# Kernel tuning notes

Hardware: AMD Instinct MI355X
Metric: run time of the kernel (lower is better)

Reference implementation:

```python
import jax, jax.numpy as jnp
import numpy as np

T = 32400   # bs*H*W BEV queries (1*180*180)
S = 16896   # bs*num_cams*h*w image keys (1*6*32*88)
E = 256     # embed_dim
H = 8       # num_heads
D = 32      # head_dim
MAXL = 32   # max interval length (ref_num_f)


def _mlp(x, w1, b1, w2, b2):
    # nn.Sequential(Linear(E,2E), ReLU, Linear(2E,E))
    return jax.nn.relu(x @ w1 + b1) @ w2 + b2


def setup_inputs() -> dict:
    k0 = jax.random.key(0)
    ks = jax.random.split(k0, 8)
    # ragged interval structure: every BEV cell has an interval of length (idx%32)+1
    lengths = (np.arange(T) % MAXL) + 1
    starts = np.concatenate([np.zeros(1, np.int64), np.cumsum(lengths)[:-1]])
    N = int(lengths.sum())  # 534472 frustum points
    ranks_bev = np.repeat(np.arange(T), lengths)          # sorted by BEV cell
    rng = np.random.default_rng(0)
    ranks_feat = rng.integers(0, S, size=N)               # which key/value row each point reads

    def lin(k, fi, fo):
        return jax.random.normal(k, (fi, fo), jnp.float32) * (1.0 / np.sqrt(fi))

    key_feat = jax.random.normal(ks[1], (S, E), jnp.float32)
    return dict(
        query_depth=jax.random.normal(ks[0], (T, E), jnp.float32),
        key=key_feat,
        value=key_feat,  # module asserts torch.equal(key, value)
        q_w1=lin(ks[2], E, 2 * E), q_b1=jnp.zeros((2 * E,), jnp.float32),
        q_w2=lin(ks[3], 2 * E, E), q_b2=jnp.zeros((E,), jnp.float32),
        k_w1=lin(ks[4], E, 2 * E), k_b1=jnp.zeros((2 * E,), jnp.float32),
        k_w2=lin(ks[5], 2 * E, E), k_b2=jnp.zeros((E,), jnp.float32),
        ranks_feat_f=jnp.asarray(ranks_feat, jnp.int32),
        ranks_bev_f=jnp.asarray(ranks_bev, jnp.int32),
        interval_starts_f=jnp.asarray(starts, jnp.int32),
        interval_lengths_f=jnp.asarray(lengths, jnp.int32),
        ref_num=MAXL,
    )


def reference(query_depth, key, value,
              q_w1, q_b1, q_w2, q_b2,
              k_w1, k_b1, k_w2, k_b2,
              ranks_feat_f, ranks_bev_f,
              interval_starts_f, interval_lengths_f, ref_num):
    scaling = 1.0 / jnp.sqrt(jnp.float32(D))
    q = (_mlp(query_depth, q_w1, q_b1, q_w2, q_b2) * scaling).reshape(T, H, D)
    k = _mlp(key, k_w1, k_b1, k_w2, k_b2).reshape(S, H, D)
    v = value.reshape(S, H, D)

    N = ranks_bev_f.shape[0]
    pt = jnp.arange(N, dtype=jnp.int32)
    # interval id of each point (intervals are contiguous, sorted by start)
    iid = jnp.searchsorted(interval_starts_f, pt, side='right') - 1
    ranks_ref = pt - interval_starts_f[iid]  # within-interval slot, in [0, ref_num)

    # per-point raw attention logit: q[bev] . k[feat] per head  -> [N, H]
    w = jnp.einsum('nhd,nhd->nh', q[ranks_bev_f], k[ranks_feat_f])

    # scatter into ragged weight tensor [T, H, ref_num]; padding masked to -1e9
    attn = jnp.full((T, H, ref_num), -1e9, jnp.float32)
    attn = attn.at[ranks_bev_f, :, ranks_ref].set(w)
    attn = jax.nn.softmax(attn, axis=-1)

    # gather normalized weights back per point and scatter-combine values
    wp = attn[ranks_bev_f, :, ranks_ref]          # [N, H]
    vp = v[ranks_feat_f]                          # [N, H, D]
    out = jnp.zeros((T, H, D), jnp.float32).at[ranks_bev_f].add(wp[:, :, None] * vp)
    return out.reshape(T, E)
```

## Files before the change

### kernel.cpp

```cpp
#include <hip/hip_runtime.h>
#include <hip/hip_bf16.h>
#include <cstdint>
#include <cstddef>

constexpr int T_Q   = 32400;
constexpr int T_PAD = 32512;
constexpr int S_K   = 16896;
constexpr int E_DIM = 256;
constexpr int HID   = 512;

typedef __bf16 bf16x8 __attribute__((ext_vector_type(8)));
typedef float  f32x4  __attribute__((ext_vector_type(4)));
typedef unsigned short ushort8v __attribute__((ext_vector_type(8)));

__device__ __forceinline__ void async16(const __hip_bfloat16* gp, __hip_bfloat16* lp) {
    __builtin_amdgcn_global_load_lds(
        (const __attribute__((address_space(1))) void*)(gp),
        (__attribute__((address_space(3))) void*)(lp), 16, 0, 0);
}

__device__ __forceinline__ float b2f(unsigned short u) {
    return __uint_as_float(((unsigned)u) << 16);
}

constexpr int NB_K = (S_K * E_DIM / 4) / 256;
constexpr int NB_PREP = NB_K + 128;

__global__ __launch_bounds__(256) void prep(
    const float* __restrict__ val_in,
    const float* __restrict__ s0, const float* __restrict__ s1,
    const float* __restrict__ s2, const float* __restrict__ s3,
    __hip_bfloat16* __restrict__ kvB,
    __hip_bfloat16* __restrict__ d0, __hip_bfloat16* __restrict__ d1,
    __hip_bfloat16* __restrict__ d2, __hip_bfloat16* __restrict__ d3) {
    __shared__ float tb[64][65];
    const int b = blockIdx.x;
    const int tid = threadIdx.x;

    if (b < NB_K) {
        int i = (b * 256 + tid) * 4;
        float4 f = *(const float4*)(val_in + i);
        union { ushort4 u4; __hip_bfloat16 bb[4]; } cv;
        cv.bb[0] = __float2bfloat16(f.x);
        cv.bb[1] = __float2bfloat16(f.y);
        cv.bb[2] = __float2bfloat16(f.z);
        cv.bb[3] = __float2bfloat16(f.w);
        int r = i >> 8, c = i & 255;
        *(ushort4*)(kvB + (size_t)r * 512 + 256 + c) = cv.u4;
        return;
    }

    int tloc = b - NB_K;
    int m = tloc >> 5;
    int tt = tloc & 31;
    const float* S = m == 0 ? s0 : m == 1 ? s1 : m == 2 ? s2 : s3;
    __hip_bfloat16* D = m == 0 ? d0 : m == 1 ? d1 : m == 2 ? d2 : d3;
    int Kd, Nd, kt, nt;
    if ((m & 1) == 0) { Kd = 256; Nd = 512; kt = tt & 3; nt = tt >> 2; }
    else              { Kd = 512; Nd = 256; kt = tt & 7; nt = tt >> 3; }
    int tx = tid & 63, ty = tid >> 6;
#pragma unroll
    for (int p = 0; p < 16; ++p) {
        int row = ty * 16 + p;
        tb[row][tx] = S[(size_t)(kt * 64 + row) * Nd + nt * 64 + tx];
    }
    __syncthreads();
#pragma unroll
    for (int p = 0; p < 16; ++p) {
        int row = ty * 16 + p;
        D[(size_t)(nt * 64 + row) * Kd + kt * 64 + tx] = __float2bfloat16(tb[tx][row]);
    }
}


constexpr int MLP_QT = T_PAD / 64;
constexpr int MLP_KT = S_K / 64;
constexpr int MLP_NB = MLP_QT + MLP_KT;

__global__ __launch_bounds__(512) void mlp_fused(
    const float* __restrict__ Aq, const float* __restrict__ Ak,
    const __hip_bfloat16* __restrict__ W1q, const __hip_bfloat16* __restrict__ W1k,
    const __hip_bfloat16* __restrict__ W2q, const __hip_bfloat16* __restrict__ W2k,
    const float* __restrict__ b1q, const float* __restrict__ b1k,
    const float* __restrict__ b2q, const float* __restrict__ b2k,
    __hip_bfloat16* __restrict__ Cq, __hip_bfloat16* __restrict__ Ck,
    float scaleq, int qtiles) {
    __shared__ __hip_bfloat16 As[64 * 256];
    __shared__ __hip_bfloat16 Bs[256 * 64];
    __shared__ __hip_bfloat16 Hs[64 * 512];

    const int b = blockIdx.x;
    const bool isq = b < qtiles;
    const float* A  = isq ? Aq : Ak;
    const __hip_bfloat16* W1 = isq ? W1q : W1k;
    const __hip_bfloat16* W2 = isq ? W2q : W2k;
    const float* b1 = isq ? b1q : b1k;
    const float* b2 = isq ? b2q : b2k;
    __hip_bfloat16* C = isq ? Cq : Ck;
    const int ldc = isq ? E_DIM : 512;
    const float scale = isq ? scaleq : 1.0f;
    const int mrow0 = (isq ? b : b - qtiles) * 64;
    const int rowlim = isq ? T_Q : S_K;

    const int tid = threadIdx.x;
    const int w = tid >> 6, l = tid & 63;
    const int lm = l & 15, lq = l >> 4;
    const int wm = w >> 2;
    const int wn4 = w & 3;
    const int srow8 = l >> 3;
    const int u8 = l & 7;
    const int scolB = (u8 ^ srow8) << 3;

#pragma unroll
    for (int c = 0; c < 4; ++c) {
        int idx = tid + c * 512;
        int row = idx >> 5;
        int u = idx & 31;
        int gr = mrow0 + row;
        float4 f0 = make_float4(0.f, 0.f, 0.f, 0.f);
        float4 f1 = make_float4(0.f, 0.f, 0.f, 0.f);
        if (gr < rowlim) {
            const float* ap = A + (size_t)gr * 256 + u * 8;
            f0 = *(const float4*)ap;
            f1 = *(const float4*)(ap + 4);
        }
        union { bf16x8 v; __hip_bfloat16 bb[8]; } cv;
        cv.bb[0] = __float2bfloat16(f0.x); cv.bb[1] = __float2bfloat16(f0.y);
        cv.bb[2] = __float2bfloat16(f0.z); cv.bb[3] = __float2bfloat16(f0.w);
        cv.bb[4] = __float2bfloat16(f1.x); cv.bb[5] = __float2bfloat16(f1.y);
        cv.bb[6] = __float2bfloat16(f1.z); cv.bb[7] = __float2bfloat16(f1.w);
        int pu = (u & 24) | ((u & 7) ^ (row & 7));
        *(bf16x8*)(As + row * 256 + pu * 8) = cv.v;
    }

#pragma unroll 1
    for (int nh = 0; nh < 2; ++nh) {
        f32x4 acc[2][4] = {};
        for (int k0 = 0; k0 < 256; k0 += 64) {
#pragma unroll
            for (int c = 0; c < 4; ++c) {
                int r = w * 32 + c * 8 + srow8;
                async16(W1 + (size_t)(nh * 256 + r) * 256 + k0 + scolB,
                        Bs + (w * 32 + c * 8) * 64);
            }
            __syncthreads();
#pragma unroll
            for (int ks = 0; ks < 2; ++ks) {
                bf16x8 af[2], bfr[4];
#pragma unroll
                for (int mi = 0; mi < 2; ++mi) {
                    int row = wm * 32 + mi * 16 + lm;
                    int un = (k0 >> 3) + ks * 4 + lq;
                    int pu = (un & 24) | ((un & 7) ^ (row & 7));
                    af[mi] = *(const bf16x8*)(As + row * 256 + pu * 8);
                }
#pragma unroll
                for (int ni = 0; ni < 4; ++ni) {
                    int brow = wn4 * 64 + ni * 16 + lm;
                    int pu = (ks * 4 + lq) ^ (brow & 7);
                    bfr[ni] = *(const bf16x8*)(Bs + brow * 64 + pu * 8);
                }
#pragma unroll
                for (int mi = 0; mi < 2; ++mi)
#pragma unroll
                    for (int ni = 0; ni < 4; ++ni)
                        acc[mi][ni] = __builtin_amdgcn_mfma_f32_16x16x32_bf16(
                            af[mi], bfr[ni], acc[mi][ni], 0, 0, 0);
            }
            __syncthreads();
        }
#pragma unroll
        for (int ni = 0; ni < 4; ++ni) {
            int col = nh * 256 + wn4 * 64 + ni * 16 + lm;
            float bv = b1[col];
            int un = col >> 3, el = col & 7;
#pragma unroll
            for (int mi = 0; mi < 2; ++mi) {
#pragma unroll
                for (int r = 0; r < 4; ++r) {
                    int row = wm * 32 + mi * 16 + lq * 4 + r;
                    float vv = fmaxf(acc[mi][ni][r] + bv, 0.f);
                    int pu = (un & 56) | ((un & 7) ^ (row & 7));
                    Hs[row * 512 + pu * 8 + el] = __float2bfloat16(vv);
                }
            }
        }
    }

    f32x4 acc2[2][4] = {};
    for (int k0 = 0; k0 < 512; k0 += 64) {
#pragma unroll
        for (int c = 0; c < 4; ++c) {
            int r = w * 32 + c * 8 + srow8;
            async16(W2 + (size_t)r * 512 + k0 + scolB,
                    Bs + (w * 32 + c * 8) * 64);
        }
        __syncthreads();
#pragma unroll
        for (int ks = 0; ks < 2; ++ks) {
            bf16x8 af[2], bfr[4];
#pragma unroll
            for (int mi = 0; mi < 2; ++mi) {
                int row = wm * 32 + mi * 16 + lm;
                int un = (k0 >> 3) + ks * 4 + lq;
                int pu = (un & 56) | ((un & 7) ^ (row & 7));
                af[mi] = *(const bf16x8*)(Hs + row * 512 + pu * 8);
            }
#pragma unroll
            for (int ni = 0; ni < 4; ++ni) {
                int brow = wn4 * 64 + ni * 16 + lm;
                int pu = (ks * 4 + lq) ^ (brow & 7);
                bfr[ni] = *(const bf16x8*)(Bs + brow * 64 + pu * 8);
            }
#pragma unroll
            for (int mi = 0; mi < 2; ++mi)
#pragma unroll
                for (int ni = 0; ni < 4; ++ni)
                    acc2[mi][ni] = __builtin_amdgcn_mfma_f32_16x16x32_bf16(
                        af[mi], bfr[ni], acc2[mi][ni], 0, 0, 0);
        }
        __syncthreads();
    }

#pragma unroll
    for (int ni = 0; ni < 4; ++ni) {
        int col = wn4 * 64 + ni * 16 + lm;
        float bv = b2[col];
#pragma unroll
        for (int mi = 0; mi < 2; ++mi) {
            size_t rowb = (size_t)mrow0 + wm * 32 + mi * 16 + lq * 4;
#pragma unroll
            for (int r = 0; r < 4; ++r) {
                float vv = (acc2[mi][ni][r] + bv) * scale;
                C[(rowb + r) * ldc + col] = __float2bfloat16(vv);
            }
        }
    }
}


#define PREFP(KB, VB, C)                                                     \
    {                                                                        \
        int f_ = __shfl(myf, (C) + half);                                    \
        const __hip_bfloat16* p_ = kv + ((size_t)f_ << 9) + (sub << 3);      \
        KB = *(const ushort8v*)p_;                                           \
        VB = *(const ushort8v*)(p_ + 256);                                   \
    }

#define PROCP(KB, VB, C)                                                     \
    {                                                                        \
        float wv = 0.f;                                                      \
        _Pragma("unroll") for (int i = 0; i < 8; ++i)                        \
            wv = fmaf(qf[i], b2f(KB[i]), wv);                                \
        wv += __shfl_xor(wv, 1);                                             \
        wv += __shfl_xor(wv, 2);                                             \
        float sc = ((C) + half < L) ? wv : -1e30f;                           \
        float so = __shfl_xor(sc, 32);                                       \
        float pm = fmaxf(sc, so);                                            \
        if (__all(pm <= m)) {                                                \
            float p = __expf(sc - m);                                        \
            s += p;                                                          \
            _Pragma("unroll") for (int i = 0; i < 8; ++i)                    \
                a[i] = fmaf(p, b2f(VB[i]), a[i]);                            \
        } else {                                                             \
            float mn = fmaxf(m, pm);                                         \
            float al = __expf(m - mn);                                       \
            float p  = __expf(sc - mn);                                      \
            m = mn;                                                          \
            s = fmaf(s, al, p);                                              \
            _Pragma("unroll") for (int i = 0; i < 8; ++i)                    \
                a[i] = fmaf(p, b2f(VB[i]), a[i] * al);                       \
        }                                                                    \
    }

#define STEPP(KB, VB, J)                                                     \
    if (c + (J) < L) {                                                       \
        PROCP(KB, VB, c + (J));                                              \
        if (c + (J) + 8 < L) PREFP(KB, VB, c + (J) + 8);                     \
    }

constexpr int ATTN_BLOCKS = 2026;

__global__ __launch_bounds__(256) void attn_kernel(
    const __hip_bfloat16* __restrict__ q,
    const __hip_bfloat16* __restrict__ kv,
    const int* __restrict__ rf,
    const int* __restrict__ starts,
    const int* __restrict__ lens,
    float* __restrict__ out) {
    const int wid = threadIdx.x >> 6;
    const int l = threadIdx.x & 63;
    const int sub = l & 31, half = l >> 5;
    const int tstride = gridDim.x * 4;

    for (int t = blockIdx.x * 4 + wid; t < T_Q; t += tstride) {
        int su = __builtin_amdgcn_readfirstlane(starts[t]);
        int L  = __builtin_amdgcn_readfirstlane(lens[t]);

        int li = l < L - 1 ? l : L - 1;
        int myf = rf[su + li];

        ushort8v qu = *(const ushort8v*)(q + (size_t)t * 256 + sub * 8);
        float qf[8];
#pragma unroll
        for (int i = 0; i < 8; ++i) qf[i] = b2f(qu[i]);

        float m = -INFINITY, s = 0.f;
        float a[8] = {0.f, 0.f, 0.f, 0.f, 0.f, 0.f, 0.f, 0.f};

        ushort8v k0 = {}, v0 = {}, k1 = {}, v1 = {};
        ushort8v k2 = {}, v2 = {}, k3 = {}, v3 = {};
        PREFP(k0, v0, 0);
        if (L > 2) PREFP(k1, v1, 2);
        if (L > 4) PREFP(k2, v2, 4);
        if (L > 6) PREFP(k3, v3, 6);

        for (int c = 0; c < L; c += 8) {
            STEPP(k0, v0, 0)
            STEPP(k1, v1, 2)
            STEPP(k2, v2, 4)
            STEPP(k3, v3, 6)
        }

        float st = s + __shfl_xor(s, 32);
#pragma unroll
        for (int i = 0; i < 8; ++i) a[i] += __shfl_xor(a[i], 32);

        if (half) {
            float inv = 1.f / st;
            float* op = out + (size_t)t * 256 + sub * 8;
            float4 o0, o1;
            o0.x = a[0] * inv; o0.y = a[1] * inv; o0.z = a[2] * inv; o0.w = a[3] * inv;
            o1.x = a[4] * inv; o1.y = a[5] * inv; o1.z = a[6] * inv; o1.w = a[7] * inv;
            *(float4*)op = o0;
            *(float4*)(op + 4) = o1;
        }
    }
}

extern "C" void kernel_launch(void* const* d_in, const int* in_sizes, int n_in,
                              void* d_out, int out_size, void* d_ws, size_t ws_size,
                              hipStream_t stream) {
    const float* q_in   = (const float*)d_in[0];
    const float* key_in = (const float*)d_in[1];
    const float* val_in = (const float*)d_in[2];
    const float* q_w1   = (const float*)d_in[3];
    const float* q_b1   = (const float*)d_in[4];
    const float* q_w2   = (const float*)d_in[5];
    const float* q_b2   = (const float*)d_in[6];
    const float* k_w1   = (const float*)d_in[7];
    const float* k_b1   = (const float*)d_in[8];
    const float* k_w2   = (const float*)d_in[9];
    const float* k_b2   = (const float*)d_in[10];
    const int* ranks_feat = (const int*)d_in[11];
    const int* starts     = (const int*)d_in[13];
    const int* lens       = (const int*)d_in[14];
    float* out = (float*)d_out;

    char* ws = (char*)d_ws;
    size_t off = 0;
    auto alloc = [&](size_t bytes) {
        char* p = ws + off;
        off += (bytes + 255) & ~(size_t)255;
        return p;
    };
    __hip_bfloat16* qMl  = (__hip_bfloat16*)alloc((size_t)T_PAD * E_DIM * 2);
    __hip_bfloat16* kvB  = (__hip_bfloat16*)alloc((size_t)S_K * 512 * 2);
    __hip_bfloat16* w1qT = (__hip_bfloat16*)alloc((size_t)HID * E_DIM * 2);
    __hip_bfloat16* w2qT = (__hip_bfloat16*)alloc((size_t)E_DIM * HID * 2);
    __hip_bfloat16* w1kT = (__hip_bfloat16*)alloc((size_t)HID * E_DIM * 2);
    __hip_bfloat16* w2kT = (__hip_bfloat16*)alloc((size_t)E_DIM * HID * 2);
    (void)ws_size; (void)n_in; (void)out_size; (void)in_sizes;

    prep<<<NB_PREP, 256, 0, stream>>>(val_in, q_w1, q_w2, k_w1, k_w2,
                                      kvB, w1qT, w2qT, w1kT, w2kT);

    const float qscale = 0.17677669529663687f;

    mlp_fused<<<MLP_NB, 512, 0, stream>>>(
        q_in, key_in, w1qT, w1kT, w2qT, w2kT,
        q_b1, k_b1, q_b2, k_b2, qMl, kvB, qscale, MLP_QT);

    attn_kernel<<<ATTN_BLOCKS, 256, 0, stream>>>(qMl, kvB, ranks_feat, starts, lens, out);
}
```

Measured before the change: 269.6 us.

## Shrink MLP shared memory by streaming A slabs and interleaving hidden halves

```diff
diff --git a/kernel.cpp b/kernel.cpp
--- a/kernel.cpp
+++ b/kernel.cpp
@@ -77,7 +77,7 @@
 constexpr int MLP_KT = S_K / 64;
 constexpr int MLP_NB = MLP_QT + MLP_KT;
 
-__global__ __launch_bounds__(512) void mlp_fused(
+__global__ __launch_bounds__(512, 4) void mlp_fused(
     const float* __restrict__ Aq, const float* __restrict__ Ak,
     const __hip_bfloat16* __restrict__ W1q, const __hip_bfloat16* __restrict__ W1k,
     const __hip_bfloat16* __restrict__ W2q, const __hip_bfloat16* __restrict__ W2k,
@@ -85,9 +85,9 @@
     const float* __restrict__ b2q, const float* __restrict__ b2k,
     __hip_bfloat16* __restrict__ Cq, __hip_bfloat16* __restrict__ Ck,
     float scaleq, int qtiles) {
-    __shared__ __hip_bfloat16 As[64 * 256];
-    __shared__ __hip_bfloat16 Bs[256 * 64];
-    __shared__ __hip_bfloat16 Hs[64 * 512];
+    __shared__ __align__(16) __hip_bfloat16 Aslab[64 * 64];
+    __shared__ __align__(16) __hip_bfloat16 Bs[256 * 64];
+    __shared__ __align__(16) __hip_bfloat16 Hs[64 * 256];
 
     const int b = blockIdx.x;
     const bool isq = b < qtiles;
@@ -109,34 +109,34 @@
     const int wn4 = w & 3;
     const int srow8 = l >> 3;
     const int u8 = l & 7;
+    const int pu8 = u8 ^ srow8;
     const int scolB = (u8 ^ srow8) << 3;
 
-#pragma unroll
-    for (int c = 0; c < 4; ++c) {
-        int idx = tid + c * 512;
-        int row = idx >> 5;
-        int u = idx & 31;
-        int gr = mrow0 + row;
-        float4 f0 = make_float4(0.f, 0.f, 0.f, 0.f);
-        float4 f1 = make_float4(0.f, 0.f, 0.f, 0.f);
-        if (gr < rowlim) {
-            const float* ap = A + (size_t)gr * 256 + u * 8;
-            f0 = *(const float4*)ap;
-            f1 = *(const float4*)(ap + 4);
-        }
-        union { bf16x8 v; __hip_bfloat16 bb[8]; } cv;
-        cv.bb[0] = __float2bfloat16(f0.x); cv.bb[1] = __float2bfloat16(f0.y);
-        cv.bb[2] = __float2bfloat16(f0.z); cv.bb[3] = __float2bfloat16(f0.w);
-        cv.bb[4] = __float2bfloat16(f1.x); cv.bb[5] = __float2bfloat16(f1.y);
-        cv.bb[6] = __float2bfloat16(f1.z); cv.bb[7] = __float2bfloat16(f1.w);
-        int pu = (u & 24) | ((u & 7) ^ (row & 7));
-        *(bf16x8*)(As + row * 256 + pu * 8) = cv.v;
-    }
+    f32x4 acc2[2][4] = {};
 
 #pragma unroll 1
     for (int nh = 0; nh < 2; ++nh) {
         f32x4 acc[2][4] = {};
-        for (int k0 = 0; k0 < 256; k0 += 64) {
+#pragma unroll 1
+        for (int st = 0; st < 4; ++st) {
+            const int k0 = st * 64;
+            {
+                int r = w * 8 + srow8;
+                int gr = mrow0 + r;
+                float4 f0 = make_float4(0.f, 0.f, 0.f, 0.f);
+                float4 f1 = make_float4(0.f, 0.f, 0.f, 0.f);
+                if (gr < rowlim) {
+                    const float* ap = A + (size_t)gr * 256 + k0 + u8 * 8;
+                    f0 = *(const float4*)ap;
+                    f1 = *(const float4*)(ap + 4);
+                }
+                union { bf16x8 v; __hip_bfloat16 bb[8]; } cv;
+                cv.bb[0] = __float2bfloat16(f0.x); cv.bb[1] = __float2bfloat16(f0.y);
+                cv.bb[2] = __float2bfloat16(f0.z); cv.bb[3] = __float2bfloat16(f0.w);
+                cv.bb[4] = __float2bfloat16(f1.x); cv.bb[5] = __float2bfloat16(f1.y);
+                cv.bb[6] = __float2bfloat16(f1.z); cv.bb[7] = __float2bfloat16(f1.w);
+                *(bf16x8*)(Aslab + r * 64 + pu8 * 8) = cv.v;
+            }
 #pragma unroll
             for (int c = 0; c < 4; ++c) {
                 int r = w * 32 + c * 8 + srow8;
@@ -150,9 +150,8 @@
 #pragma unroll
                 for (int mi = 0; mi < 2; ++mi) {
                     int row = wm * 32 + mi * 16 + lm;
-                    int un = (k0 >> 3) + ks * 4 + lq;
-                    int pu = (un & 24) | ((un & 7) ^ (row & 7));
-                    af[mi] = *(const bf16x8*)(As + row * 256 + pu * 8);
+                    int pu = (ks * 4 + lq) ^ (row & 7);
+                    af[mi] = *(const bf16x8*)(Aslab + row * 64 + pu * 8);
                 }
 #pragma unroll
                 for (int ni = 0; ni < 4; ++ni) {
@@ -169,10 +168,11 @@
             }
             __syncthreads();
         }
+
 #pragma unroll
         for (int ni = 0; ni < 4; ++ni) {
-            int col = nh * 256 + wn4 * 64 + ni * 16 + lm;
-            float bv = b1[col];
+            int col = wn4 * 64 + ni * 16 + lm;
+            float bv = b1[nh * 256 + col];
             int un = col >> 3, el = col & 7;
 #pragma unroll
             for (int mi = 0; mi < 2; ++mi) {
@@ -180,46 +180,47 @@
                 for (int r = 0; r < 4; ++r) {
                     int row = wm * 32 + mi * 16 + lq * 4 + r;
                     float vv = fmaxf(acc[mi][ni][r] + bv, 0.f);
-                    int pu = (un & 56) | ((un & 7) ^ (row & 7));
-                    Hs[row * 512 + pu * 8 + el] = __float2bfloat16(vv);
-                }
-            }
-        }
-    }
-
-    f32x4 acc2[2][4] = {};
-    for (int k0 = 0; k0 < 512; k0 += 64) {
-#pragma unroll
-        for (int c = 0; c < 4; ++c) {
-            int r = w * 32 + c * 8 + srow8;
-            async16(W2 + (size_t)r * 512 + k0 + scolB,
-                    Bs + (w * 32 + c * 8) * 64);
-        }
-        __syncthreads();
-#pragma unroll
-        for (int ks = 0; ks < 2; ++ks) {
-            bf16x8 af[2], bfr[4];
-#pragma unroll
-            for (int mi = 0; mi < 2; ++mi) {
-                int row = wm * 32 + mi * 16 + lm;
-                int un = (k0 >> 3) + ks * 4 + lq;
-                int pu = (un & 56) | ((un & 7) ^ (row & 7));
-                af[mi] = *(const bf16x8*)(Hs + row * 512 + pu * 8);
-            }
-#pragma unroll
-            for (int ni = 0; ni < 4; ++ni) {
-                int brow = wn4 * 64 + ni * 16 + lm;
-                int pu = (ks * 4 + lq) ^ (brow & 7);
-                bfr[ni] = *(const bf16x8*)(Bs + brow * 64 + pu * 8);
-            }
-#pragma unroll
-            for (int mi = 0; mi < 2; ++mi)
-#pragma unroll
-                for (int ni = 0; ni < 4; ++ni)
-                    acc2[mi][ni] = __builtin_amdgcn_mfma_f32_16x16x32_bf16(
-                        af[mi], bfr[ni], acc2[mi][ni], 0, 0, 0);
-        }
-        __syncthreads();
+                    int pu = (un & 24) | ((un & 7) ^ (row & 7));
+                    Hs[row * 256 + pu * 8 + el] = __float2bfloat16(vv);
+                }
+            }
+        }
+
+#pragma unroll 1
+        for (int st = 0; st < 4; ++st) {
+            const int k0 = st * 64;
+#pragma unroll
+            for (int c = 0; c < 4; ++c) {
+                int r = w * 32 + c * 8 + srow8;
+                async16(W2 + (size_t)r * 512 + nh * 256 + k0 + scolB,
+                        Bs + (w * 32 + c * 8) * 64);
+            }
+            __syncthreads();
+#pragma unroll
+            for (int ks = 0; ks < 2; ++ks) {
+                bf16x8 af[2], bfr[4];
+#pragma unroll
+                for (int mi = 0; mi < 2; ++mi) {
+                    int row = wm * 32 + mi * 16 + lm;
+                    int un = st * 8 + ks * 4 + lq;
+                    int pu = (un & 24) | ((un & 7) ^ (row & 7));
+                    af[mi] = *(const bf16x8*)(Hs + row * 256 + pu * 8);
+                }
+#pragma unroll
+                for (int ni = 0; ni < 4; ++ni) {
+                    int brow = wn4 * 64 + ni * 16 + lm;
+                    int pu = (ks * 4 + lq) ^ (brow & 7);
+                    bfr[ni] = *(const bf16x8*)(Bs + brow * 64 + pu * 8);
+                }
+#pragma unroll
+                for (int mi = 0; mi < 2; ++mi)
+#pragma unroll
+                    for (int ni = 0; ni < 4; ++ni)
+                        acc2[mi][ni] = __builtin_amdgcn_mfma_f32_16x16x32_bf16(
+                            af[mi], bfr[ni], acc2[mi][ni], 0, 0, 0);
+            }
+            __syncthreads();
+        }
     }
 
 #pragma unroll
```

After: 273.4 us. No clear change (+1.4%).
